# Performance work log

Hardware: AMD Instinct MI355X
Metric: run time of the kernel (lower is better)

## Reference

```python
import jax, jax.numpy as jnp
import numpy as np

EPS = 0.001  # epsilon used by both custom layer norms in the source
B, T, D, H, O = 64, 1024, 128, 256, 64


def setup_inputs() -> dict:
    key = jax.random.key(0)
    ks = jax.random.split(key, 8)
    s = 0.05
    return {
        "x": jax.random.normal(ks[0], (B, T, D), jnp.float32),
        "Wi": jax.random.normal(ks[1], (4 * H, D), jnp.float32) * s,   # input_weights
        "bi": jax.random.normal(ks[2], (4 * H,), jnp.float32) * s,
        "Wh": jax.random.normal(ks[3], (4 * H, H), jnp.float32) * s,   # hidden_weights
        "bh": jax.random.normal(ks[4], (4 * H,), jnp.float32) * s,
        "lna_gamma": jnp.ones((4 * H,), jnp.float32),
        "lna_beta": jnp.zeros((4 * H,), jnp.float32),
        "ln_gamma": jnp.ones((H,), jnp.float32),
        "ln_beta": jnp.zeros((H,), jnp.float32),
        "Wf": jax.random.normal(ks[5], (O, H), jnp.float32) * s,       # fc
        "bf": jax.random.normal(ks[6], (O,), jnp.float32) * s,
    }


def _ln(x, gamma, beta):
    # custom layer norm: mean/var over last axis, eps=1e-3 (no Bessel correction)
    m = jnp.mean(x, axis=-1, keepdims=True)
    xs = x - m
    v = jnp.mean(xs * xs, axis=-1, keepdims=True)
    return gamma * (xs / jnp.sqrt(v + EPS)) + beta


def reference(x, Wi, bi, Wh, bh, lna_gamma, lna_beta, ln_gamma, ln_beta, Wf, bf):
    b, t, d = x.shape
    h = Wh.shape[1]
    # precompute input projections for all timesteps: (T, B, 4H)
    xproj = jnp.einsum('btd,gd->tbg', x, Wi) + bi

    def step(carry, xp_t):
        hx, cx = carry                              # (B, H) each
        gates = xp_t + hx @ Wh.T + bh               # (B, 4H)
        # layer_norm_all: normalize each of the 4 gate blocks over H
        g4 = gates.reshape(b, 4, h)
        m = jnp.mean(g4, axis=-1, keepdims=True)
        gs = g4 - m
        v = jnp.mean(gs * gs, axis=-1, keepdims=True)
        gates = (gs / jnp.sqrt(v + EPS)).reshape(b, 4 * h) * lna_gamma + lna_beta
        ig, fg, cg, og = jnp.split(gates, 4, axis=1)
        ig = jax.nn.sigmoid(ig)
        fg = jax.nn.sigmoid(fg)
        cg = jnp.tanh(cg)
        og = jax.nn.sigmoid(og)
        cy = fg * cx + ig * cg
        hy = og * jnp.tanh(_ln(cy, ln_gamma, ln_beta))
        return (hy, cy), hy

    h0 = jnp.zeros((b, h), x.dtype)
    c0 = jnp.zeros((b, h), x.dtype)
    _, hs = jax.lax.scan(step, (h0, c0), xproj)     # hs: (T, B, H)
    out = hs.transpose(1, 0, 2)                     # (B, T, H)
    yhat = jax.nn.relu(out @ Wf.T + bf)             # (B, T, O)
    return yhat
```

## Files before the change

kernel.cpp:

```cpp
#include <hip/hip_runtime.h>

#define T_TOT 1024
#define BB 64
#define DD 128
#define HH 256
#define GG 1024
#define OO 64
#define LN_EPS 1e-3f
#define NV 23
#define NL 9

typedef unsigned int u32;
typedef _Float16 h2 __attribute__((ext_vector_type(2)));

__device__ __forceinline__ float fdot2(u32 a, u32 b, float c) {
  return __builtin_amdgcn_fdot2(__builtin_bit_cast(h2, a), __builtin_bit_cast(h2, b), c, false);
}
__device__ __forceinline__ u32 pkf16(float lo, float hi) {
  h2 v = { (_Float16)lo, (_Float16)hi };
  return __builtin_bit_cast(u32, v);
}
__device__ __forceinline__ float fast_sigmoid(float x) { return 1.0f / (1.0f + __expf(-x)); }
__device__ __forceinline__ float fast_tanh(float x) { return 2.0f / (1.0f + __expf(-2.0f * x)) - 1.0f; }

__global__ void prep_wh(const float* __restrict__ Wh, uint4* __restrict__ whp4) {
  int id = blockIdx.x * 256 + threadIdx.x;
  int kb = id >> 10, g = id & 1023;
  const float* p = Wh + (size_t)g * HH + kb * 8;
  uint4 o;
  o.x = pkf16(p[0], p[1]); o.y = pkf16(p[2], p[3]);
  o.z = pkf16(p[4], p[5]); o.w = pkf16(p[6], p[7]);
  whp4[id] = o;
}

__global__ void prep_wi(const float* __restrict__ Wi, uint4* __restrict__ wip4) {
  int id = blockIdx.x * 256 + threadIdx.x;
  int kp4 = id >> 10, g = id & 1023;
  const float* p = Wi + (size_t)g * DD + kp4 * 8;
  uint4 o;
  o.x = pkf16(p[0], p[1]); o.y = pkf16(p[2], p[3]);
  o.z = pkf16(p[4], p[5]); o.w = pkf16(p[6], p[7]);
  wip4[id] = o;
}

__global__ __launch_bounds__(256) void xproj_gemm(
    const float* __restrict__ x, const uint4* __restrict__ wip4,
    const float* __restrict__ bi, const float* __restrict__ bh,
    _Float16* __restrict__ xph, int m0) {
  __shared__ _Float16 xl[16][128];
  const int tid = threadIdx.x;
  const int mt = blockIdx.x, gt = blockIdx.y;
  const int g = gt * 256 + tid;
#pragma unroll
  for (int i = 0; i < 8; ++i) {
    int idx = i * 256 + tid;
    int p = idx >> 7, d = idx & 127;
    int m = m0 + mt * 16 + p;
    xl[p][d] = (_Float16)x[(size_t)(m & 63) * (T_TOT * DD) + (size_t)(m >> 6) * DD + d];
  }
  __syncthreads();
  float acc[16];
#pragma unroll
  for (int p = 0; p < 16; ++p) acc[p] = 0.f;
#pragma unroll
  for (int kp4 = 0; kp4 < 16; ++kp4) {
    uint4 w = wip4[kp4 * GG + g];
#pragma unroll
    for (int p = 0; p < 16; ++p) {
      uint4 hv = *(const uint4*)(&xl[p][kp4 * 8]);
      acc[p] = fdot2(w.x, hv.x, acc[p]);
      acc[p] = fdot2(w.y, hv.y, acc[p]);
      acc[p] = fdot2(w.z, hv.z, acc[p]);
      acc[p] = fdot2(w.w, hv.w, acc[p]);
    }
  }
  float bsum = bi[g] + bh[g];
#pragma unroll
  for (int p = 0; p < 16; ++p) {
    int ml = mt * 16 + p;
    xph[(size_t)ml * GG + g] = (_Float16)(acc[p] + bsum);
  }
}

__global__ __attribute__((amdgpu_flat_work_group_size(512, 512), amdgpu_waves_per_eu(2, 2)))
void lstm_scan(
    const uint4* __restrict__ whp4, const _Float16* __restrict__ xph,
    const float* __restrict__ lna_g, const float* __restrict__ lna_b,
    const float* __restrict__ ln_g, const float* __restrict__ ln_b,
    _Float16* __restrict__ hs16,
    _Float16* __restrict__ hxst, float* __restrict__ cxst,
    int t0, int ct) {
  extern __shared__ char smem[];
  uint4* wl = (uint4*)smem;
  _Float16* hx16 = (_Float16*)(smem + 147456);
  float* red  = (float*)(smem + 147968);
  float* red2 = (float*)(smem + 148032);
  float* gact = (float*)(smem + 148064);

  const int tid = threadIdx.x;
  const int b = blockIdx.x;
  const int lane = tid & 63, wid = tid >> 6;
  const int q = wid >> 1, r = wid & 1;
  const int gA = q * 256 + r * 128 + lane;
  const int gB = gA + 64;

  uint4 wrA[NV], wrB[NV];
#pragma unroll
  for (int kb = 0; kb < NV; ++kb) {
    wrA[kb] = whp4[kb * 1024 + gA];
    wrB[kb] = whp4[kb * 1024 + gB];
  }
#pragma unroll
  for (int j = 0; j < NL; ++j) {
    wl[j * 512 + tid]        = whp4[(NV + j) * 1024 + gA];
    wl[(NL + j) * 512 + tid] = whp4[(NV + j) * 1024 + gB];
  }
  float lgA = lna_g[gA], lbA = lna_b[gA];
  float lgB = lna_g[gB], lbB = lna_b[gB];
  float lng = 0.f, lnb = 0.f, cx = 0.f;
  if (tid < HH) {
    lng = ln_g[tid]; lnb = ln_b[tid];
    if (t0 == 0) {
      hx16[tid] = (_Float16)0.f;
    } else {
      hx16[tid] = hxst[b * HH + tid]; cx = cxst[b * HH + tid];
    }
  }
  __syncthreads();

  const _Float16* xrA = xph + b * GG + gA;
  const _Float16* xrB = xph + b * GG + gB;
  _Float16* hsp = hs16 + (size_t)b * HH + (tid & 255);

  _Float16 xA16 = xrA[0], xB16 = xrB[0];
  for (int tl = 0; tl < ct; ++tl) {
    float accA = (float)xA16, accB = (float)xB16;
    if (tl + 1 < ct) {
      xA16 = xrA[(size_t)(tl + 1) * (BB * GG)];
      xB16 = xrB[(size_t)(tl + 1) * (BB * GG)];
    }
#pragma unroll
    for (int kb = 0; kb < NV; ++kb) {
      uint4 hv = *(const uint4*)(hx16 + kb * 8);
      accA = fdot2(wrA[kb].x, hv.x, accA);
      accA = fdot2(wrA[kb].y, hv.y, accA);
      accA = fdot2(wrA[kb].z, hv.z, accA);
      accA = fdot2(wrA[kb].w, hv.w, accA);
      accB = fdot2(wrB[kb].x, hv.x, accB);
      accB = fdot2(wrB[kb].y, hv.y, accB);
      accB = fdot2(wrB[kb].z, hv.z, accB);
      accB = fdot2(wrB[kb].w, hv.w, accB);
    }
#pragma unroll
    for (int j = 0; j < NL; ++j) {
      uint4 hv = *(const uint4*)(hx16 + (NV + j) * 8);
      uint4 wA = wl[j * 512 + tid];
      uint4 wB = wl[(NL + j) * 512 + tid];
      accA = fdot2(wA.x, hv.x, accA);
      accA = fdot2(wA.y, hv.y, accA);
      accA = fdot2(wA.z, hv.z, accA);
      accA = fdot2(wA.w, hv.w, accA);
      accB = fdot2(wB.x, hv.x, accB);
      accB = fdot2(wB.y, hv.y, accB);
      accB = fdot2(wB.z, hv.z, accB);
      accB = fdot2(wB.w, hv.w, accB);
    }

    float s = accA + accB, ss = accA * accA + accB * accB;
#pragma unroll
    for (int m = 1; m <= 32; m <<= 1) {
      s += __shfl_xor(s, m, 64);
      ss += __shfl_xor(ss, m, 64);
    }
    if (lane == 0) { red[wid] = s; red[8 + wid] = ss; }
    __syncthreads();
    float S  = red[2 * q] + red[2 * q + 1];
    float SS = red[8 + 2 * q] + red[8 + 2 * q + 1];
    float mean = S * (1.f / HH);
    float var = SS * (1.f / HH) - mean * mean;
    float rstd = rsqrtf(var + LN_EPS);
    float gnA = (accA - mean) * rstd * lgA + lbA;
    float gnB = (accB - mean) * rstd * lgB + lbB;
    float avA, avB;
    if (q == 2) { avA = fast_tanh(gnA); avB = fast_tanh(gnB); }
    else        { avA = fast_sigmoid(gnA); avB = fast_sigmoid(gnB); }
    gact[gA] = avA; gact[gB] = avB;
    __syncthreads();

    float cy = 0.f;
    if (tid < HH) {
      int h = tid;
      cy = gact[HH + h] * cx + gact[h] * gact[2 * HH + h];
      cx = cy;
      float s2 = cy, ss2 = cy * cy;
#pragma unroll
      for (int m = 1; m <= 32; m <<= 1) {
        s2 += __shfl_xor(s2, m, 64);
        ss2 += __shfl_xor(ss2, m, 64);
      }
      if (lane == 0) { red2[wid] = s2; red2[4 + wid] = ss2; }
    }
    __syncthreads();
    if (tid < HH) {
      int h = tid;
      float S2  = red2[0] + red2[1] + red2[2] + red2[3];
      float SS2 = red2[4] + red2[5] + red2[6] + red2[7];
      float mc = S2 * (1.f / HH);
      float vc = SS2 * (1.f / HH) - mc * mc;
      float cyn = (cy - mc) * rsqrtf(vc + LN_EPS) * lng + lnb;
      float hy = gact[3 * HH + h] * fast_tanh(cyn);
      hx16[h] = (_Float16)hy;
      hsp[(size_t)(t0 + tl) * (BB * HH)] = (_Float16)hy;
    }
    __syncthreads();
  }
  if (tid < HH) { hxst[b * HH + tid] = hx16[tid]; cxst[b * HH + tid] = cx; }
}

__global__ __launch_bounds__(256) void out_gemm(
    const _Float16* __restrict__ hs16, const float* __restrict__ Wf,
    const float* __restrict__ bf, float* __restrict__ out) {
  __shared__ u32 wfl[128][64];
  __shared__ u32 hsl[16][132];
  const int tid = threadIdx.x;
  const int mbase = blockIdx.x * 16;
#pragma unroll
  for (int i = 0; i < 32; ++i) {
    int idx = i * 256 + tid;
    int kp = idx >> 6, o = idx & 63;
    wfl[kp][o] = pkf16(Wf[o * HH + kp * 2], Wf[o * HH + kp * 2 + 1]);
  }
#pragma unroll
  for (int i = 0; i < 8; ++i) {
    int idx = i * 256 + tid;
    int p = idx >> 7, kp = idx & 127;
    hsl[p][kp] = *(const u32*)(hs16 + (size_t)(mbase + p) * HH + kp * 2);
  }
  __syncthreads();
  const int o = tid & 63, mi = tid >> 6;
  float bfo = bf[o];
#pragma unroll
  for (int mm = mi; mm < 16; mm += 4) {
    float a0 = bfo, a1 = 0.f, a2 = 0.f, a3 = 0.f;
#pragma unroll
    for (int kp = 0; kp < 128; kp += 4) {
      a0 = fdot2(wfl[kp + 0][o], hsl[mm][kp + 0], a0);
      a1 = fdot2(wfl[kp + 1][o], hsl[mm][kp + 1], a1);
      a2 = fdot2(wfl[kp + 2][o], hsl[mm][kp + 2], a2);
      a3 = fdot2(wfl[kp + 3][o], hsl[mm][kp + 3], a3);
    }
    float r = (a0 + a1) + (a2 + a3);
    int m = mbase + mm;
    out[(size_t)(m & 63) * (T_TOT * OO) + (size_t)(m >> 6) * OO + o] = fmaxf(r, 0.f);
  }
}

extern "C" void kernel_launch(void* const* d_in, const int* in_sizes, int n_in,
                              void* d_out, int out_size, void* d_ws, size_t ws_size,
                              hipStream_t stream) {
  if (n_in < 11) return;
  const float* x    = (const float*)d_in[0];
  const float* Wi   = (const float*)d_in[1];
  const float* bi   = (const float*)d_in[2];
  const float* Wh   = (const float*)d_in[3];
  const float* bh   = (const float*)d_in[4];
  const float* lnag = (const float*)d_in[5];
  const float* lnab = (const float*)d_in[6];
  const float* lng  = (const float*)d_in[7];
  const float* lnb  = (const float*)d_in[8];
  const float* Wf   = (const float*)d_in[9];
  const float* bf   = (const float*)d_in[10];
  float* out = (float*)d_out;

  char* ws = (char*)d_ws;
  uint4* whp4 = (uint4*)ws;
  uint4* wip4 = (uint4*)(ws + (512 << 10));
  _Float16* hs16 = (_Float16*)(ws + (1 << 20));
  _Float16* hxst = (_Float16*)(ws + (1 << 20) + (32 << 20));
  float* cxst = (float*)(ws + (1 << 20) + (32 << 20) + (64 << 10));
  const size_t xph_off = (size_t)35 << 20;
  _Float16* xph = (_Float16*)(ws + xph_off);

  size_t avail = ws_size > xph_off ? ws_size - xph_off : 0;
  int ct = T_TOT;
  while (ct > 1 && (size_t)ct * (BB * GG * 2) > avail) ct >>= 1;

  const int scan_smem = 152160;
  (void)hipFuncSetAttribute(reinterpret_cast<const void*>(lstm_scan),
                            hipFuncAttributeMaxDynamicSharedMemorySize, scan_smem);

  prep_wh<<<128, 256, 0, stream>>>(Wh, whp4);
  prep_wi<<<64, 256, 0, stream>>>(Wi, wip4);
  for (int t0 = 0; t0 < T_TOT; t0 += ct) {
    xproj_gemm<<<dim3((ct * BB) / 16, 4), 256, 0, stream>>>(x, wip4, bi, bh, xph, t0 * BB);
    lstm_scan<<<BB, 512, scan_smem, stream>>>(whp4, xph, lnag, lnab, lng, lnb,
                                              hs16, hxst, cxst, t0, ct);
  }
  out_gemm<<<(T_TOT * BB) / 16, 256, 0, stream>>>(hs16, Wf, bf, out);
}
```

Before: 3.012 ms.

## Replace fdot2 recurrent matvec with MFMA 16x16x32 using fragment-packed Wh

The recurrent h·Wh^T product in the scan kernel now runs through MFMA f16 instructions instead of per-thread fdot2 chains. Wh is prepacked into B-fragment layout, with most fragments held in registers and the rest in LDS. The input-projection output is permuted to match the MFMA result layout. Only row 0 of the A operand is non-zero because each block handles one batch row, so 15/16 of the MFMA work is wasted. This trades many dependent dot2 ops for fewer matrix ops, with extra register pressure from the f16x8 weight arrays.

```diff
diff --git a/kernel.cpp b/kernel.cpp
--- a/kernel.cpp
+++ b/kernel.cpp
@@ -7,11 +7,13 @@
 #define GG 1024
 #define OO 64
 #define LN_EPS 1e-3f
-#define NV 23
-#define NL 9
+#define NBR 45
+#define NBL 19
 
 typedef unsigned int u32;
 typedef _Float16 h2 __attribute__((ext_vector_type(2)));
+typedef _Float16 f16x8 __attribute__((ext_vector_type(8)));
+typedef float f32x4 __attribute__((ext_vector_type(4)));
 
 __device__ __forceinline__ float fdot2(u32 a, u32 b, float c) {
   return __builtin_amdgcn_fdot2(__builtin_bit_cast(h2, a), __builtin_bit_cast(h2, b), c, false);
@@ -23,14 +25,17 @@
 __device__ __forceinline__ float fast_sigmoid(float x) { return 1.0f / (1.0f + __expf(-x)); }
 __device__ __forceinline__ float fast_tanh(float x) { return 2.0f / (1.0f + __expf(-2.0f * x)) - 1.0f; }
 
-__global__ void prep_wh(const float* __restrict__ Wh, uint4* __restrict__ whp4) {
+__global__ void prep_bfrag(const float* __restrict__ Wh, uint4* __restrict__ bfragG) {
   int id = blockIdx.x * 256 + threadIdx.x;
-  int kb = id >> 10, g = id & 1023;
-  const float* p = Wh + (size_t)g * HH + kb * 8;
+  int lane = id & 63, tile = (id >> 6) & 63, w = id >> 12;
+  int t = tile >> 3, n = tile & 7;
+  int col = w * 128 + n * 16 + (lane & 15);
+  int k0 = t * 32 + (lane >> 4) * 8;
+  const float* p = Wh + (size_t)col * HH + k0;
   uint4 o;
   o.x = pkf16(p[0], p[1]); o.y = pkf16(p[2], p[3]);
   o.z = pkf16(p[4], p[5]); o.w = pkf16(p[6], p[7]);
-  whp4[id] = o;
+  bfragG[id] = o;
 }
 
 __global__ void prep_wi(const float* __restrict__ Wi, uint4* __restrict__ wip4) {
@@ -51,6 +56,7 @@
   const int tid = threadIdx.x;
   const int mt = blockIdx.x, gt = blockIdx.y;
   const int g = gt * 256 + tid;
+  const int woff = ((g >> 7) << 7) | ((g & 15) << 3) | ((g >> 4) & 7);
 #pragma unroll
   for (int i = 0; i < 8; ++i) {
     int idx = i * 256 + tid;
@@ -78,45 +84,44 @@
 #pragma unroll
   for (int p = 0; p < 16; ++p) {
     int ml = mt * 16 + p;
-    xph[(size_t)ml * GG + g] = (_Float16)(acc[p] + bsum);
+    xph[(size_t)ml * GG + woff] = (_Float16)(acc[p] + bsum);
   }
 }
 
 __global__ __attribute__((amdgpu_flat_work_group_size(512, 512), amdgpu_waves_per_eu(2, 2)))
 void lstm_scan(
-    const uint4* __restrict__ whp4, const _Float16* __restrict__ xph,
+    const uint4* __restrict__ bfragG, const _Float16* __restrict__ xphf,
     const float* __restrict__ lna_g, const float* __restrict__ lna_b,
     const float* __restrict__ ln_g, const float* __restrict__ ln_b,
     _Float16* __restrict__ hs16,
     _Float16* __restrict__ hxst, float* __restrict__ cxst,
     int t0, int ct) {
   extern __shared__ char smem[];
-  uint4* wl = (uint4*)smem;
-  _Float16* hx16 = (_Float16*)(smem + 147456);
-  float* red  = (float*)(smem + 147968);
-  float* red2 = (float*)(smem + 148032);
-  float* gact = (float*)(smem + 148064);
-
-  const int tid = threadIdx.x;
-  const int b = blockIdx.x;
-  const int lane = tid & 63, wid = tid >> 6;
-  const int q = wid >> 1, r = wid & 1;
-  const int gA = q * 256 + r * 128 + lane;
-  const int gB = gA + 64;
-
-  uint4 wrA[NV], wrB[NV];
-#pragma unroll
-  for (int kb = 0; kb < NV; ++kb) {
-    wrA[kb] = whp4[kb * 1024 + gA];
-    wrB[kb] = whp4[kb * 1024 + gB];
-  }
-#pragma unroll
-  for (int j = 0; j < NL; ++j) {
-    wl[j * 512 + tid]        = whp4[(NV + j) * 1024 + gA];
-    wl[(NL + j) * 512 + tid] = whp4[(NV + j) * 1024 + gB];
-  }
-  float lgA = lna_g[gA], lbA = lna_b[gA];
-  float lgB = lna_g[gB], lbB = lna_b[gB];
+  f16x8* wl = (f16x8*)smem;
+  _Float16* hx16 = (_Float16*)(smem + 155648);
+  float* red  = (float*)(smem + 156160);
+  float* red2 = (float*)(smem + 156224);
+  float* gact = (float*)(smem + 156256);
+
+  const int tid = threadIdx.x, b = blockIdx.x;
+  const int lane = tid & 63, wid = tid >> 6, q = wid >> 1;
+  const int l4 = lane & 15;
+
+  const uint4* bw = bfragG + wid * 4096;
+  f16x8 breg[NBR];
+#pragma unroll
+  for (int i = 0; i < NBR; ++i) breg[i] = __builtin_bit_cast(f16x8, bw[i * 64 + lane]);
+#pragma unroll
+  for (int i = NBR; i < 64; ++i)
+    wl[(wid * NBL + (i - NBR)) * 64 + lane] = __builtin_bit_cast(f16x8, bw[i * 64 + lane]);
+
+  u32 lgp[4], lbp[4];
+#pragma unroll
+  for (int k = 0; k < 4; ++k) {
+    int g0 = wid * 128 + (2 * k) * 16 + l4;
+    lgp[k] = pkf16(lna_g[g0], lna_g[g0 + 16]);
+    lbp[k] = pkf16(lna_b[g0], lna_b[g0 + 16]);
+  }
   float lng = 0.f, lnb = 0.f, cx = 0.f;
   if (tid < HH) {
     lng = ln_g[tid]; lnb = ln_b[tid];
@@ -128,47 +133,42 @@
   }
   __syncthreads();
 
-  const _Float16* xrA = xph + b * GG + gA;
-  const _Float16* xrB = xph + b * GG + gB;
+  const _Float16* xrow = xphf + (size_t)b * GG + wid * 128 + l4 * 8;
   _Float16* hsp = hs16 + (size_t)b * HH + (tid & 255);
 
-  _Float16 xA16 = xrA[0], xB16 = xrB[0];
+  f16x8 xp = *(const f16x8*)xrow;
   for (int tl = 0; tl < ct; ++tl) {
-    float accA = (float)xA16, accB = (float)xB16;
-    if (tl + 1 < ct) {
-      xA16 = xrA[(size_t)(tl + 1) * (BB * GG)];
-      xB16 = xrB[(size_t)(tl + 1) * (BB * GG)];
-    }
-#pragma unroll
-    for (int kb = 0; kb < NV; ++kb) {
-      uint4 hv = *(const uint4*)(hx16 + kb * 8);
-      accA = fdot2(wrA[kb].x, hv.x, accA);
-      accA = fdot2(wrA[kb].y, hv.y, accA);
-      accA = fdot2(wrA[kb].z, hv.z, accA);
-      accA = fdot2(wrA[kb].w, hv.w, accA);
-      accB = fdot2(wrB[kb].x, hv.x, accB);
-      accB = fdot2(wrB[kb].y, hv.y, accB);
-      accB = fdot2(wrB[kb].z, hv.z, accB);
-      accB = fdot2(wrB[kb].w, hv.w, accB);
-    }
-#pragma unroll
-    for (int j = 0; j < NL; ++j) {
-      uint4 hv = *(const uint4*)(hx16 + (NV + j) * 8);
-      uint4 wA = wl[j * 512 + tid];
-      uint4 wB = wl[(NL + j) * 512 + tid];
-      accA = fdot2(wA.x, hv.x, accA);
-      accA = fdot2(wA.y, hv.y, accA);
-      accA = fdot2(wA.z, hv.z, accA);
-      accA = fdot2(wA.w, hv.w, accA);
-      accB = fdot2(wB.x, hv.x, accB);
-      accB = fdot2(wB.y, hv.y, accB);
-      accB = fdot2(wB.z, hv.z, accB);
-      accB = fdot2(wB.w, hv.w, accB);
-    }
-
-    float s = accA + accB, ss = accA * accA + accB * accB;
-#pragma unroll
-    for (int m = 1; m <= 32; m <<= 1) {
+    f32x4 acc[8];
+#pragma unroll
+    for (int n = 0; n < 8; ++n) acc[n] = (f32x4){0.f, 0.f, 0.f, 0.f};
+#pragma unroll
+    for (int t = 0; t < 8; ++t) {
+      uint4 hv = *(const uint4*)(hx16 + t * 32 + ((lane >> 4) << 3));
+      uint4 az;
+      az.x = (l4 == 0) ? hv.x : 0u;
+      az.y = (l4 == 0) ? hv.y : 0u;
+      az.z = (l4 == 0) ? hv.z : 0u;
+      az.w = (l4 == 0) ? hv.w : 0u;
+      f16x8 afr = __builtin_bit_cast(f16x8, az);
+#pragma unroll
+      for (int n = 0; n < 8; ++n) {
+        const int idx = t * 8 + n;
+        f16x8 bfr;
+        if (idx < NBR) bfr = breg[idx];
+        else           bfr = wl[(wid * NBL + (idx - NBR)) * 64 + lane];
+        acc[n] = __builtin_amdgcn_mfma_f32_16x16x32_f16(afr, bfr, acc[n], 0, 0, 0);
+      }
+    }
+    float g8[8];
+#pragma unroll
+    for (int n = 0; n < 8; ++n) g8[n] = acc[n][0] + (float)xp[n];
+    if (tl + 1 < ct) xp = *(const f16x8*)(xrow + (size_t)(tl + 1) * (BB * GG));
+
+    float s = 0.f, ss = 0.f;
+#pragma unroll
+    for (int n = 0; n < 8; ++n) { s += g8[n]; ss += g8[n] * g8[n]; }
+#pragma unroll
+    for (int m = 1; m <= 8; m <<= 1) {
       s += __shfl_xor(s, m, 64);
       ss += __shfl_xor(ss, m, 64);
     }
@@ -179,12 +179,16 @@
     float mean = S * (1.f / HH);
     float var = SS * (1.f / HH) - mean * mean;
     float rstd = rsqrtf(var + LN_EPS);
-    float gnA = (accA - mean) * rstd * lgA + lbA;
-    float gnB = (accB - mean) * rstd * lgB + lbB;
-    float avA, avB;
-    if (q == 2) { avA = fast_tanh(gnA); avB = fast_tanh(gnB); }
-    else        { avA = fast_sigmoid(gnA); avB = fast_sigmoid(gnB); }
-    gact[gA] = avA; gact[gB] = avB;
+    if (lane < 16) {
+#pragma unroll
+      for (int n = 0; n < 8; ++n) {
+        h2 lgv = __builtin_bit_cast(h2, lgp[n >> 1]);
+        h2 lbv = __builtin_bit_cast(h2, lbp[n >> 1]);
+        float gn = (g8[n] - mean) * rstd * (float)lgv[n & 1] + (float)lbv[n & 1];
+        float av = (q == 2) ? fast_tanh(gn) : fast_sigmoid(gn);
+        gact[wid * 128 + n * 16 + lane] = av;
+      }
+    }
     __syncthreads();
 
     float cy = 0.f;
@@ -273,7 +277,7 @@
   float* out = (float*)d_out;
 
   char* ws = (char*)d_ws;
-  uint4* whp4 = (uint4*)ws;
+  uint4* bfragG = (uint4*)ws;
   uint4* wip4 = (uint4*)(ws + (512 << 10));
   _Float16* hs16 = (_Float16*)(ws + (1 << 20));
   _Float16* hxst = (_Float16*)(ws + (1 << 20) + (32 << 20));
@@ -285,15 +289,15 @@
   int ct = T_TOT;
   while (ct > 1 && (size_t)ct * (BB * GG * 2) > avail) ct >>= 1;
 
-  const int scan_smem = 152160;
+  const int scan_smem = 160352;
   (void)hipFuncSetAttribute(reinterpret_cast<const void*>(lstm_scan),
                             hipFuncAttributeMaxDynamicSharedMemorySize, scan_smem);
 
-  prep_wh<<<128, 256, 0, stream>>>(Wh, whp4);
+  prep_bfrag<<<128, 256, 0, stream>>>(Wh, bfragG);
   prep_wi<<<64, 256, 0, stream>>>(Wi, wip4);
   for (int t0 = 0; t0 < T_TOT; t0 += ct) {
     xproj_gemm<<<dim3((ct * BB) / 16, 4), 256, 0, stream>>>(x, wip4, bi, bh, xph, t0 * BB);
-    lstm_scan<<<BB, 512, scan_smem, stream>>>(whp4, xph, lnag, lnab, lng, lnb,
+    lstm_scan<<<BB, 512, scan_smem, stream>>>(bfragG, xph, lnag, lnab, lng, lnb,
                                               hs16, hxst, cxst, t0, ct);
   }
   out_gemm<<<(T_TOT * BB) / 16, 256, 0, stream>>>(hs16, Wf, bf, out);
```

Result: slower. 3.610 ms (+19.8%).
